# Kernel tuning notes

Measured on AMD Instinct MI355X. Metric: run time of the kernel, lower is better.

Reference implementation:

```python
import jax, jax.numpy as jnp
import numpy as np

BINS = 32
WIN = 9
SIGMA_RATIO = 1.0
_SIGMA = (1.0 / (BINS - 1)) * SIGMA_RATIO          # mean(diff(linspace(0,1,bins)))
PRETERM = 2.0 / (2.0 * _SIGMA ** 2)                # = 961 for bins=32, ratio=1
BIN_CENTERS = jnp.linspace(0.0, 1.0, BINS)


def _correlation_ratio(X, Y, win=WIN):
    B, C, H, W, D = Y.shape
    h_r, w_r, d_r = (-H) % win, (-W) % win, (-D) % win
    pad = ((0, 0), (0, 0),
           (h_r // 2, h_r - h_r // 2),
           (w_r // 2, w_r - w_r // 2),
           (d_r // 2, d_r - d_r // 2))
    X = jnp.pad(X, pad)
    Y = jnp.pad(Y, pad)
    B, C, H, W, D = Y.shape
    nH, nW, nD = H // win, W // win, D // win
    num_patch = nH * nW * nD

    def to_flat(T):
        T = T.reshape(B, C, nH, win, nW, win, nD, win)
        return T.transpose(0, 2, 4, 6, 1, 3, 5, 7).reshape(B * num_patch, C, win ** 3)

    x_flat = to_flat(X)                              # [P, C, w3]
    y_flat = to_flat(Y)                              # [P, C, w3]

    bins = BIN_CENTERS.astype(Y.dtype)
    diff = y_flat[:, :, None, :] - bins[None, None, :, None]   # [P, C, bins, w3]
    weights = jnp.exp(-PRETERM * jnp.square(diff))              # Parzen Gaussian
    weights_norm = weights / (jnp.sum(weights, axis=-1, keepdims=True) + 1e-5)

    mean_intensities = jnp.sum(weights_norm * x_flat[:, :, None, :], axis=3)  # [P, C, bins]
    bin_counts = jnp.sum(weights, axis=3)                                     # [P, C, bins]
    total_mean = jnp.mean(x_flat, axis=2, keepdims=True)                      # [P, C, 1]

    between_group_variance = (
        jnp.sum(bin_counts * (mean_intensities - total_mean) ** 2, axis=2)
        / jnp.sum(bin_counts, axis=2)
    )                                                                          # [P, C]
    total_variance = jnp.var(x_flat, axis=2, ddof=1)                           # unbiased, like torch.var
    eta_square = between_group_variance / (total_variance + 1e-5)
    return jnp.mean(eta_square) / 3.0


def reference(y_true, y_pred):
    CR = _correlation_ratio(y_true, y_pred) + _correlation_ratio(y_pred, y_true)
    s = WIN // 2
    yt = jnp.roll(y_true, shift=(-s, -s, -s), axis=(2, 3, 4))
    yp = jnp.roll(y_pred, shift=(-s, -s, -s), axis=(2, 3, 4))
    CR_shifted = _correlation_ratio(yt, yp) + _correlation_ratio(yp, yt)
    return -CR / 4.0 - CR_shifted / 4.0


def setup_inputs() -> dict:
    key = jax.random.key(0)
    k1, k2 = jax.random.split(key)
    shape = (1, 1, 90, 90, 90)
    y_true = jax.random.uniform(k1, shape, dtype=jnp.float32)
    y_pred = jax.random.uniform(k2, shape, dtype=jnp.float32)
    return {"y_true": y_true, "y_pred": y_pred}
```

## Files before the change

kernel.cpp:

```cpp
#include <hip/hip_runtime.h>


constexpr int   NPATCH  = 1000;
constexpr float PRETERM = 961.0f;

__global__ __launch_bounds__(64)
void cr_patch_kernel(const float* __restrict__ yt,
                     const float* __restrict__ yp,
                     float* __restrict__ etas)
{
    const int bid  = blockIdx.x;
    const int conf = bid / NPATCH;
    const int p    = bid - conf * NPATCH;
    const int ph   = p / 100;
    const int pw   = (p / 10) % 10;
    const int pd   = p % 10;

    const float* __restrict__ X = (conf & 1) ? yp : yt;
    const float* __restrict__ Y = (conf & 1) ? yt : yp;
    const int shift = (conf >= 2) ? 4 : 0;

    const int lane = threadIdx.x;

    float xs[12], ys[12];
    float sumx = 0.f, sumx2 = 0.f;

    auto load_voxel = [&](int j, float& xv, float& yv) {
        int dh  = j / 81;
        int rem = j - dh * 81;
        int dw  = rem / 9;
        int dd  = rem - dw * 9;
        int H = ph * 9 + dh + shift; if (H >= 90) H -= 90;
        int W = pw * 9 + dw + shift; if (W >= 90) W -= 90;
        int D = pd * 9 + dd + shift; if (D >= 90) D -= 90;
        int idx = (H * 90 + W) * 90 + D;
        xv = X[idx];
        yv = Y[idx];
    };

    #pragma unroll
    for (int v = 0; v < 11; ++v) {
        load_voxel(lane + (v << 6), xs[v], ys[v]);
        sumx  += xs[v];
        sumx2  = fmaf(xs[v], xs[v], sumx2);
    }
    if (lane < 729 - 11 * 64) {
        load_voxel(lane + 704, xs[11], ys[11]);
        sumx  += xs[11];
        sumx2  = fmaf(xs[11], xs[11], sumx2);
    } else {
        xs[11] = 0.f;
        ys[11] = 10.f;
    }

    #pragma unroll
    for (int m = 1; m < 64; m <<= 1) {
        sumx  += __shfl_xor(sumx,  m);
        sumx2 += __shfl_xor(sumx2, m);
    }
    const float mean = sumx * (1.0f / 729.0f);

    const int l5 = lane & 31;
    const int hi = lane & 32;
    float r_sw = 0.f, r_swx = 0.f;

    for (int k = 0; k < 32; ++k) {
        const int   b = (l5 + k) & 31;
        const float c = (float)b * (1.0f / 31.0f);
        float sw = 0.f, swx = 0.f;
        #pragma unroll
        for (int v = 0; v < 12; ++v) {
            float d = ys[v] - c;
            float w = __expf(-PRETERM * d * d);
            sw += w;
            swx = fmaf(w, xs[v], swx);
        }
        const int src = hi | ((l5 - k) & 31);
        r_sw  += __shfl(sw,  src, 64);
        r_swx += __shfl(swx, src, 64);
    }
    r_sw  += __shfl_xor(r_sw,  32);
    r_swx += __shfl_xor(r_swx, 32);

    float mi  = r_swx / (r_sw + 1e-5f);
    float dmu = mi - mean;
    float tn  = r_sw * dmu * dmu;
    float td  = r_sw;
    #pragma unroll
    for (int m = 1; m < 32; m <<= 1) {
        tn += __shfl_xor(tn, m);
        td += __shfl_xor(td, m);
    }
    if (lane == 0) {
        float bgv = tn / td;
        float tv  = (sumx2 - sumx * sumx * (1.0f / 729.0f)) * (1.0f / 728.0f);
        etas[bid] = bgv / (tv + 1e-5f);
    }
}

__global__ __launch_bounds__(256)
void cr_reduce_kernel(const float* __restrict__ etas, float* __restrict__ out)
{
    __shared__ float red[4];
    float s = 0.f;
    for (int i = threadIdx.x; i < 4 * NPATCH; i += 256) s += etas[i];
    #pragma unroll
    for (int m = 1; m < 64; m <<= 1) s += __shfl_xor(s, m);
    if ((threadIdx.x & 63) == 0) red[threadIdx.x >> 6] = s;
    __syncthreads();
    if (threadIdx.x == 0)
        out[0] = -(red[0] + red[1] + red[2] + red[3]) * (1.0f / 12000.0f);
}

extern "C" void kernel_launch(void* const* d_in, const int* in_sizes, int n_in,
                              void* d_out, int out_size, void* d_ws, size_t ws_size,
                              hipStream_t stream)
{
    const float* y_true = (const float*)d_in[0];
    const float* y_pred = (const float*)d_in[1];
    float* out  = (float*)d_out;
    float* etas = (float*)d_ws;

    cr_patch_kernel<<<4 * NPATCH, 64, 0, stream>>>(y_true, y_pred, etas);
    cr_reduce_kernel<<<1, 256, 0, stream>>>(etas, out);
}
```

Measured before the change: 89.52 us.

## Fuse both CR directions per patch and fold final reduction via atomic counter

Result: slower. 171.9 us (+92.0%).

```diff
diff --git a/kernel.cpp b/kernel.cpp
--- a/kernel.cpp
+++ b/kernel.cpp
@@ -7,25 +7,21 @@
 __global__ __launch_bounds__(64)
 void cr_patch_kernel(const float* __restrict__ yt,
                      const float* __restrict__ yp,
-                     float* __restrict__ etas)
+                     float* __restrict__ partial,
+                     unsigned* __restrict__ cnt,
+                     float* __restrict__ out)
 {
-    const int bid  = blockIdx.x;
-    const int conf = bid / NPATCH;
-    const int p    = bid - conf * NPATCH;
-    const int ph   = p / 100;
-    const int pw   = (p / 10) % 10;
-    const int pd   = p % 10;
-
-    const float* __restrict__ X = (conf & 1) ? yp : yt;
-    const float* __restrict__ Y = (conf & 1) ? yt : yp;
-    const int shift = (conf >= 2) ? 4 : 0;
-
+    const int bid     = blockIdx.x;
+    const int shifted = (bid >= NPATCH);
+    const int p       = shifted ? bid - NPATCH : bid;
+    const int shift   = shifted ? 4 : 0;
+    const int ph = p / 100, pw = (p / 10) % 10, pd = p % 10;
     const int lane = threadIdx.x;
 
     float xs[12], ys[12];
-    float sumx = 0.f, sumx2 = 0.f;
+    float st = 0.f, st2 = 0.f, sp = 0.f, sp2 = 0.f;
 
-    auto load_voxel = [&](int j, float& xv, float& yv) {
+    auto load_voxel = [&](int j, float& tv, float& pv) {
         int dh  = j / 81;
         int rem = j - dh * 81;
         int dw  = rem / 9;
@@ -34,82 +30,91 @@
         int W = pw * 9 + dw + shift; if (W >= 90) W -= 90;
         int D = pd * 9 + dd + shift; if (D >= 90) D -= 90;
         int idx = (H * 90 + W) * 90 + D;
-        xv = X[idx];
-        yv = Y[idx];
+        tv = yt[idx];
+        pv = yp[idx];
     };
 
     #pragma unroll
     for (int v = 0; v < 11; ++v) {
         load_voxel(lane + (v << 6), xs[v], ys[v]);
-        sumx  += xs[v];
-        sumx2  = fmaf(xs[v], xs[v], sumx2);
+        st += xs[v]; st2 = fmaf(xs[v], xs[v], st2);
+        sp += ys[v]; sp2 = fmaf(ys[v], ys[v], sp2);
     }
     if (lane < 729 - 11 * 64) {
         load_voxel(lane + 704, xs[11], ys[11]);
-        sumx  += xs[11];
-        sumx2  = fmaf(xs[11], xs[11], sumx2);
+        st += xs[11]; st2 = fmaf(xs[11], xs[11], st2);
+        sp += ys[11]; sp2 = fmaf(ys[11], ys[11], sp2);
     } else {
-        xs[11] = 0.f;
-        ys[11] = 10.f;
+        xs[11] = 10.f; ys[11] = 10.f;
     }
 
     #pragma unroll
     for (int m = 1; m < 64; m <<= 1) {
-        sumx  += __shfl_xor(sumx,  m);
-        sumx2 += __shfl_xor(sumx2, m);
+        st  += __shfl_xor(st,  m);  st2 += __shfl_xor(st2, m);
+        sp  += __shfl_xor(sp,  m);  sp2 += __shfl_xor(sp2, m);
     }
-    const float mean = sumx * (1.0f / 729.0f);
+    const float meanT = st * (1.0f / 729.0f);
+    const float meanP = sp * (1.0f / 729.0f);
 
     const int l5 = lane & 31;
     const int hi = lane & 32;
-    float r_sw = 0.f, r_swx = 0.f;
+    float rA_w = 0.f, rA_wx = 0.f;
+    float rB_w = 0.f, rB_wx = 0.f;
 
     for (int k = 0; k < 32; ++k) {
         const int   b = (l5 + k) & 31;
         const float c = (float)b * (1.0f / 31.0f);
-        float sw = 0.f, swx = 0.f;
+        float aw = 0.f, awx = 0.f, bw = 0.f, bwx = 0.f;
         #pragma unroll
         for (int v = 0; v < 12; ++v) {
-            float d = ys[v] - c;
-            float w = __expf(-PRETERM * d * d);
-            sw += w;
-            swx = fmaf(w, xs[v], swx);
+            float dA = ys[v] - c;
+            float wA = __expf(-PRETERM * dA * dA);
+            aw += wA; awx = fmaf(wA, xs[v], awx);
+            float dB = xs[v] - c;
+            float wB = __expf(-PRETERM * dB * dB);
+            bw += wB; bwx = fmaf(wB, ys[v], bwx);
         }
         const int src = hi | ((l5 - k) & 31);
-        r_sw  += __shfl(sw,  src, 64);
-        r_swx += __shfl(swx, src, 64);
+        rA_w  += __shfl(aw,  src, 64);
+        rA_wx += __shfl(awx, src, 64);
+        rB_w  += __shfl(bw,  src, 64);
+        rB_wx += __shfl(bwx, src, 64);
     }
-    r_sw  += __shfl_xor(r_sw,  32);
-    r_swx += __shfl_xor(r_swx, 32);
+    rA_w += __shfl_xor(rA_w, 32);  rA_wx += __shfl_xor(rA_wx, 32);
+    rB_w += __shfl_xor(rB_w, 32);  rB_wx += __shfl_xor(rB_wx, 32);
 
-    float mi  = r_swx / (r_sw + 1e-5f);
-    float dmu = mi - mean;
-    float tn  = r_sw * dmu * dmu;
-    float td  = r_sw;
+    float miA = rA_wx / (rA_w + 1e-5f);
+    float duA = miA - meanT;
+    float tnA = rA_w * duA * duA, tdA = rA_w;
+    float miB = rB_wx / (rB_w + 1e-5f);
+    float duB = miB - meanP;
+    float tnB = rB_w * duB * duB, tdB = rB_w;
     #pragma unroll
     for (int m = 1; m < 32; m <<= 1) {
-        tn += __shfl_xor(tn, m);
-        td += __shfl_xor(td, m);
+        tnA += __shfl_xor(tnA, m);  tdA += __shfl_xor(tdA, m);
+        tnB += __shfl_xor(tnB, m);  tdB += __shfl_xor(tdB, m);
     }
     if (lane == 0) {
-        float bgv = tn / td;
-        float tv  = (sumx2 - sumx * sumx * (1.0f / 729.0f)) * (1.0f / 728.0f);
-        etas[bid] = bgv / (tv + 1e-5f);
+        float tvT = (st2 - st * st * (1.0f / 729.0f)) * (1.0f / 728.0f);
+        float tvP = (sp2 - sp * sp * (1.0f / 729.0f)) * (1.0f / 728.0f);
+        float eta = (tnA / tdA) / (tvT + 1e-5f) + (tnB / tdB) / (tvP + 1e-5f);
+        __hip_atomic_store(&partial[bid], eta, __ATOMIC_RELAXED, __HIP_MEMORY_SCOPE_AGENT);
     }
-}
 
-__global__ __launch_bounds__(256)
-void cr_reduce_kernel(const float* __restrict__ etas, float* __restrict__ out)
-{
-    __shared__ float red[4];
-    float s = 0.f;
-    for (int i = threadIdx.x; i < 4 * NPATCH; i += 256) s += etas[i];
-    #pragma unroll
-    for (int m = 1; m < 64; m <<= 1) s += __shfl_xor(s, m);
-    if ((threadIdx.x & 63) == 0) red[threadIdx.x >> 6] = s;
-    __syncthreads();
-    if (threadIdx.x == 0)
-        out[0] = -(red[0] + red[1] + red[2] + red[3]) * (1.0f / 12000.0f);
+    __threadfence();
+    unsigned old = 0;
+    if (lane == 0)
+        old = __hip_atomic_fetch_add(cnt, 1u, __ATOMIC_ACQ_REL, __HIP_MEMORY_SCOPE_AGENT);
+    old = __shfl(old, 0, 64);
+    if (old == 2u * NPATCH - 1u) {
+        __threadfence();
+        float s = 0.f;
+        for (int i = lane; i < 2 * NPATCH; i += 64)
+            s += __hip_atomic_load(&partial[i], __ATOMIC_RELAXED, __HIP_MEMORY_SCOPE_AGENT);
+        #pragma unroll
+        for (int m = 1; m < 64; m <<= 1) s += __shfl_xor(s, m);
+        if (lane == 0) out[0] = -s * (1.0f / 12000.0f);
+    }
 }
 
 extern "C" void kernel_launch(void* const* d_in, const int* in_sizes, int n_in,
@@ -118,9 +123,10 @@
 {
     const float* y_true = (const float*)d_in[0];
     const float* y_pred = (const float*)d_in[1];
-    float* out  = (float*)d_out;
-    float* etas = (float*)d_ws;
+    float*    out     = (float*)d_out;
+    float*    partial = (float*)d_ws;
+    unsigned* cnt     = (unsigned*)((char*)d_ws + 8192);
 
-    cr_patch_kernel<<<4 * NPATCH, 64, 0, stream>>>(y_true, y_pred, etas);
-    cr_reduce_kernel<<<1, 256, 0, stream>>>(etas, out);
+    hipMemsetAsync(cnt, 0, sizeof(unsigned), stream);
+    cr_patch_kernel<<<2 * NPATCH, 64, 0, stream>>>(y_true, y_pred, partial, cnt, out);
 }
```
